# Optimization experiments

Measured on AMD Instinct MI355X. Metric: run time of the kernel, lower is better.

## Reference

```python
import jax, jax.numpy as jnp
import numpy as np

NEG_SLOPE = 0.01  # F.leaky_relu / nn.LeakyReLU default

def _leaky(x):
    return jnp.where(x >= 0, x, NEG_SLOPE * x)

def _cgconv(x, src, dst, edge_attr, Wf, bf, Ws, bs):
    # PyG CGConv: z = [x_i, x_j, e]; msg = sigmoid(lin_f(z)) * softplus(lin_s(z)); out = x + scatter_add(msg, i)
    z = jnp.concatenate([x[dst], x[src], edge_attr], axis=-1)  # [E, 2C+D]
    m = jax.nn.sigmoid(z @ Wf + bf) * jax.nn.softplus(z @ Ws + bs)  # [E, C]
    agg = jax.ops.segment_sum(m, dst, num_segments=x.shape[0])
    return x + agg

def setup_inputs() -> dict:
    key = jax.random.key(0)
    ks = jax.random.split(key, 16)
    N, E, C, D, NC, G = 50000, 800000, 128, 32, 10, 64
    inp = {}
    inp['x'] = jax.random.normal(ks[0], (N, C), dtype=jnp.float32)
    inp['y'] = jax.random.randint(ks[1], (G,), 0, NC)
    inp['edge_index'] = jax.random.randint(ks[2], (2, E), 0, N)
    inp['edge_attr'] = jax.random.normal(ks[3], (E, D), dtype=jnp.float32)
    inp['batch'] = jnp.sort(jax.random.randint(ks[4], (N,), 0, G))
    s = 0.05
    inp['lin_W'] = jax.random.normal(ks[5], (C + NC, C), dtype=jnp.float32) * s
    inp['lin_b'] = jnp.zeros((C,), dtype=jnp.float32)
    inp['c1_Wf'] = jax.random.normal(ks[6], (2 * C + D, C), dtype=jnp.float32) * s
    inp['c1_bf'] = jnp.zeros((C,), dtype=jnp.float32)
    inp['c1_Ws'] = jax.random.normal(ks[7], (2 * C + D, C), dtype=jnp.float32) * s
    inp['c1_bs'] = jnp.zeros((C,), dtype=jnp.float32)
    inp['c2_Wf'] = jax.random.normal(ks[8], (2 * C + D, C), dtype=jnp.float32) * s
    inp['c2_bf'] = jnp.zeros((C,), dtype=jnp.float32)
    inp['c2_Ws'] = jax.random.normal(ks[9], (2 * C + D, C), dtype=jnp.float32) * s
    inp['c2_bs'] = jnp.zeros((C,), dtype=jnp.float32)
    inp['fc1_W'] = jax.random.normal(ks[10], (C + NC, 32), dtype=jnp.float32) * s
    inp['fc1_b'] = jnp.zeros((32,), dtype=jnp.float32)
    inp['fc2_W'] = jax.random.normal(ks[11], (32, 1), dtype=jnp.float32) * s
    inp['fc2_b'] = jnp.zeros((1,), dtype=jnp.float32)
    return inp

def reference(x, y, edge_index, edge_attr, batch, lin_W, lin_b, c1_Wf, c1_bf, c1_Ws, c1_bs, c2_Wf, c2_bf, c2_Ws, c2_bs, fc1_W, fc1_b, fc2_W, fc2_b):
    NC = fc1_W.shape[0] - c1_Wf.shape[1]  # n_classes = 10
    G = y.shape[0]
    src, dst = edge_index[0], edge_index[1]
    one_hot = jax.nn.one_hot(y[batch], NC, dtype=x.dtype)  # [N, NC]
    h = _leaky(jnp.concatenate([x, one_hot], axis=1) @ lin_W + lin_b)
    h = _leaky(_cgconv(h, src, dst, edge_attr, c1_Wf, c1_bf, c1_Ws, c1_bs))
    h = _cgconv(h, src, dst, edge_attr, c2_Wf, c2_bf, c2_Ws, c2_bs)
    h = jnp.concatenate([h, one_hot], axis=1)  # [N, C+NC]
    sums = jax.ops.segment_sum(h, batch, num_segments=G)
    cnts = jax.ops.segment_sum(jnp.ones((h.shape[0],), h.dtype), batch, num_segments=G)
    pooled = sums / jnp.maximum(cnts, 1.0)[:, None]  # global_mean_pool
    out = _leaky(pooled @ fc1_W + fc1_b) @ fc2_W + fc2_b
    return jax.nn.sigmoid(out)
```

## Files before the change

### kernel.cpp

```cpp
#include <hip/hip_runtime.h>
#include <hip/hip_bf16.h>
#include <math.h>

#define CCH 128
#define DK  32
#define NCLS 10

typedef __attribute__((ext_vector_type(2))) float f32x2;

__device__ __forceinline__ float leaky_f(float v) { return v >= 0.f ? v : 0.01f * v; }

__global__ void k_hist(const int* __restrict__ dst, int* __restrict__ cnt, int E) {
  int e = blockIdx.x * 256 + threadIdx.x;
  if (e < E) atomicAdd(&cnt[dst[e]], 1);
}

__global__ void k_scan(const int* __restrict__ cnt, int* __restrict__ off,
                       int* __restrict__ cur, int N) {
  __shared__ int wsum[16];
  __shared__ int carry_s;
  int t = threadIdx.x;
  int lane = t & 63, w = t >> 6;
  if (t == 0) carry_s = 0;
  __syncthreads();
  for (int base = 0; base < N; base += 1024) {
    int i = base + t;
    int carry = carry_s;
    int v = (i < N) ? cnt[i] : 0;
    int s = v;
    #pragma unroll
    for (int d = 1; d < 64; d <<= 1) {
      int tmp = __shfl_up(s, d);
      if (lane >= d) s += tmp;
    }
    if (lane == 63) wsum[w] = s;
    __syncthreads();
    if (t < 16) {
      int u = wsum[t];
      #pragma unroll
      for (int d = 1; d < 16; d <<= 1) {
        int tmp = __shfl_up(u, d);
        if (t >= d) u += tmp;
      }
      wsum[t] = u;
      if (t == 15) carry_s = carry + u;
    }
    __syncthreads();
    int wbase = carry + (w > 0 ? wsum[w - 1] : 0);
    int excl = wbase + s - v;
    if (i < N) { off[i] = excl; cur[i] = excl; }
    __syncthreads();
  }
  if (t == 0) off[N] = carry_s;
}

__global__ void k_fill(const int* __restrict__ dst, const int* __restrict__ srcArr,
                       int* __restrict__ cur, int* __restrict__ eid,
                       int* __restrict__ esrc, int E) {
  int e = blockIdx.x * 256 + threadIdx.x;
  if (e < E) {
    int p = atomicAdd(&cur[dst[e]], 1);
    eid[p] = e;
    esrc[p] = srcArr[e];
  }
}

__global__ void k_gea(const int* __restrict__ eid, const float* __restrict__ ea,
                      float* __restrict__ ea_csr, int E) {
  int t = blockIdx.x * 256 + threadIdx.x;
  if (t >= E * 8) return;
  int i = t >> 3, q = t & 7;
  int e = eid[i];
  *(float4*)&ea_csr[(size_t)i * DK + q * 4] =
      *(const float4*)&ea[(size_t)e * DK + q * 4];
}

__global__ __launch_bounds__(256) void k_embed(
    const float* __restrict__ x, const float* __restrict__ lin_W,
    const float* __restrict__ lin_b, const int* __restrict__ batch,
    const int* __restrict__ y, float* __restrict__ h, int M) {
  __shared__ float Al[32 * 128];
  __shared__ float Wl[32 * 128];
  int t = threadIdx.x;
  int row0 = blockIdx.x * 32;
  for (int i = t * 4; i < 32 * 128; i += 1024) {
    int r = i >> 7, k = i & 127;
    int gr = row0 + r;
    float4 v = {0.f, 0.f, 0.f, 0.f};
    if (gr < M) v = *(const float4*)&x[(size_t)gr * 128 + k];
    *(float4*)&Al[i] = v;
  }
  int c4 = (t & 31) * 4;
  int rb = (t >> 5) * 4;
  float acc[4][4] = {};
  for (int ks = 0; ks < 128; ks += 32) {
    __syncthreads();
    for (int i = t * 4; i < 32 * 128; i += 1024)
      *(float4*)&Wl[i] = *(const float4*)&lin_W[(size_t)ks * 128 + i];
    __syncthreads();
    for (int k = 0; k < 32; k += 4) {
      float4 a[4];
      #pragma unroll
      for (int r = 0; r < 4; ++r) a[r] = *(float4*)&Al[(rb + r) * 128 + ks + k];
      #pragma unroll
      for (int kk = 0; kk < 4; ++kk) {
        float4 w = *(float4*)&Wl[(k + kk) * 128 + c4];
        #pragma unroll
        for (int r = 0; r < 4; ++r) {
          float av = kk == 0 ? a[r].x : kk == 1 ? a[r].y : kk == 2 ? a[r].z : a[r].w;
          acc[r][0] = fmaf(av, w.x, acc[r][0]);
          acc[r][1] = fmaf(av, w.y, acc[r][1]);
          acc[r][2] = fmaf(av, w.z, acc[r][2]);
          acc[r][3] = fmaf(av, w.w, acc[r][3]);
        }
      }
    }
  }
  #pragma unroll
  for (int r = 0; r < 4; ++r) {
    int gr = row0 + rb + r;
    if (gr < M) {
      int cls = y[batch[gr]];
      const float* wrow = &lin_W[(size_t)(128 + cls) * 128];
      float4 o;
      o.x = leaky_f(acc[r][0] + lin_b[c4 + 0] + wrow[c4 + 0]);
      o.y = leaky_f(acc[r][1] + lin_b[c4 + 1] + wrow[c4 + 1]);
      o.z = leaky_f(acc[r][2] + lin_b[c4 + 2] + wrow[c4 + 2]);
      o.w = leaky_f(acc[r][3] + lin_b[c4 + 3] + wrow[c4 + 3]);
      *(float4*)&h[(size_t)gr * 128 + c4] = o;
    }
  }
}

__global__ __launch_bounds__(256) void k_proj(
    const float* __restrict__ h, const float* __restrict__ Wf,
    const float* __restrict__ Ws, float* __restrict__ P, int M) {
  __shared__ float Al[32 * 128];
  __shared__ float Wl[32 * 128];
  int t = threadIdx.x;
  int part = blockIdx.y;
  const float* Wsrc = (part < 2 ? Wf : Ws) + (size_t)(part & 1) * (128 * 128);
  int row0 = blockIdx.x * 32;
  for (int i = t * 4; i < 32 * 128; i += 1024) {
    int r = i >> 7, k = i & 127;
    int gr = row0 + r;
    float4 v = {0.f, 0.f, 0.f, 0.f};
    if (gr < M) v = *(const float4*)&h[(size_t)gr * 128 + k];
    *(float4*)&Al[i] = v;
  }
  int c4 = (t & 31) * 4;
  int rb = (t >> 5) * 4;
  float acc[4][4] = {};
  for (int ks = 0; ks < 128; ks += 32) {
    __syncthreads();
    for (int i = t * 4; i < 32 * 128; i += 1024)
      *(float4*)&Wl[i] = *(const float4*)&Wsrc[(size_t)ks * 128 + i];
    __syncthreads();
    for (int k = 0; k < 32; k += 4) {
      float4 a[4];
      #pragma unroll
      for (int r = 0; r < 4; ++r) a[r] = *(float4*)&Al[(rb + r) * 128 + ks + k];
      #pragma unroll
      for (int kk = 0; kk < 4; ++kk) {
        float4 w = *(float4*)&Wl[(k + kk) * 128 + c4];
        #pragma unroll
        for (int r = 0; r < 4; ++r) {
          float av = kk == 0 ? a[r].x : kk == 1 ? a[r].y : kk == 2 ? a[r].z : a[r].w;
          acc[r][0] = fmaf(av, w.x, acc[r][0]);
          acc[r][1] = fmaf(av, w.y, acc[r][1]);
          acc[r][2] = fmaf(av, w.z, acc[r][2]);
          acc[r][3] = fmaf(av, w.w, acc[r][3]);
        }
      }
    }
  }
  #pragma unroll
  for (int r = 0; r < 4; ++r) {
    int gr = row0 + rb + r;
    if (gr < M) {
      float4 o = {acc[r][0], acc[r][1], acc[r][2], acc[r][3]};
      *(float4*)&P[(size_t)gr * 512 + part * 128 + c4] = o;
    }
  }
}

__global__ __launch_bounds__(256) __attribute__((amdgpu_waves_per_eu(3, 3)))
void k_agg(
    const float* __restrict__ hin, const float* __restrict__ P,
    const int* __restrict__ off,
    const int* __restrict__ esrcArr, const float* __restrict__ ea_csr,
    const float* __restrict__ Wf, const float* __restrict__ Ws,
    const float* __restrict__ bfv, const float* __restrict__ bsv,
    float* __restrict__ hout, int N, int do_leaky) {
  int lane = threadIdx.x & 63;
  int wave = __builtin_amdgcn_readfirstlane(threadIdx.x >> 6);
  int gw = blockIdx.x * 4 + wave;
  int c2 = lane * 2;
  f32x2 wf[DK], ws[DK];
  #pragma unroll
  for (int k = 0; k < DK; ++k) {
    wf[k] = *(const f32x2*)&Wf[(size_t)(256 + k) * 128 + c2];
    ws[k] = *(const f32x2*)&Ws[(size_t)(256 + k) * 128 + c2];
  }
  f32x2 bf2 = *(const f32x2*)&bfv[c2];
  f32x2 bs2 = *(const f32x2*)&bsv[c2];
  int nstreams = gridDim.x * 4;
  for (int n = gw; n < N; n += nstreams) {
    int i0 = __builtin_amdgcn_readfirstlane(off[n]);
    int i1 = __builtin_amdgcn_readfirstlane(off[n + 1]);
    f32x2 acc = *(const f32x2*)&hin[(size_t)n * 128 + c2];
    f32x2 gf0 = *(const f32x2*)&P[(size_t)n * 512 + c2] + bf2;
    f32x2 gs0 = *(const f32x2*)&P[(size_t)n * 512 + 256 + c2] + bs2;
    #pragma unroll 1
    for (int i = i0; i < i1; ++i) {
      int s = __builtin_amdgcn_readfirstlane(esrcArr[i]);
      f32x2 gf = gf0 + *(const f32x2*)&P[(size_t)s * 512 + 128 + c2];
      f32x2 gs = gs0 + *(const f32x2*)&P[(size_t)s * 512 + 384 + c2];
      const float4* ep4 = (const float4*)(ea_csr + (size_t)i * DK);
      #pragma unroll
      for (int q = 0; q < 4; ++q) {
        float4 a = ep4[2 * q];
        float4 b = ep4[2 * q + 1];
        float ekk[8] = {a.x, a.y, a.z, a.w, b.x, b.y, b.z, b.w};
        #pragma unroll
        for (int j = 0; j < 8; ++j) {
          int k = q * 8 + j;
          f32x2 e2 = {ekk[j], ekk[j]};
          gf += e2 * wf[k];
          gs += e2 * ws[k];
        }
      }
      float sgx = 1.f / (1.f + __expf(-gf.x));
      float sgy = 1.f / (1.f + __expf(-gf.y));
      float spx = fmaxf(gs.x, 0.f) + __logf(1.f + __expf(-fabsf(gs.x)));
      float spy = fmaxf(gs.y, 0.f) + __logf(1.f + __expf(-fabsf(gs.y)));
      acc.x = fmaf(sgx, spx, acc.x);
      acc.y = fmaf(sgy, spy, acc.y);
    }
    if (do_leaky) { acc.x = leaky_f(acc.x); acc.y = leaky_f(acc.y); }
    *(f32x2*)&hout[(size_t)n * 128 + c2] = acc;
  }
}

__device__ __forceinline__ int lbound(const int* a, int n, int key) {
  int lo = 0, hi = n;
  while (lo < hi) { int m = (lo + hi) >> 1; if (a[m] < key) lo = m + 1; else hi = m; }
  return lo;
}

__global__ void k_pool(const float* __restrict__ h, const int* __restrict__ batch,
                       float* __restrict__ pooled, int* __restrict__ gcnt, int N) {
  int g = blockIdx.x;
  int sidx = blockIdx.y, sgrid = gridDim.y;
  int t = threadIdx.x;
  int lo = lbound(batch, N, g);
  int hi = lbound(batch, N, g + 1);
  int len = hi - lo;
  if (sidx == 0 && t == 0) gcnt[g] = len;
  int per = (len + sgrid - 1) / sgrid;
  int a = lo + sidx * per;
  int b = min(hi, a + per);
  if (a >= b) return;
  float s = 0.f;
  for (int n = a; n < b; ++n) s += h[(size_t)n * 128 + t];
  atomicAdd(&pooled[g * 128 + t], s);
}

__global__ void k_fc(const float* __restrict__ pooled, const int* __restrict__ gcnt,
                     const int* __restrict__ y,
                     const float* __restrict__ W1, const float* __restrict__ b1,
                     const float* __restrict__ W2, const float* __restrict__ b2,
                     float* __restrict__ out) {
  int g = blockIdx.x;
  int j = threadIdx.x;
  float v = 0.f;
  if (j < 32) {
    int cnt = gcnt[g];
    float dot = 0.f;
    for (int k = 0; k < 128; ++k) dot = fmaf(pooled[g * 128 + k], W1[k * 32 + j], dot);
    float a = b1[j] + (cnt > 0 ? dot / (float)cnt + W1[(128 + y[g]) * 32 + j] : 0.f);
    a = leaky_f(a);
    v = a * W2[j];
  }
  #pragma unroll
  for (int o = 32; o > 0; o >>= 1) v += __shfl_down(v, o);
  if (j == 0) out[g] = 1.f / (1.f + __expf(-(v + b2[0])));
}

extern "C" void kernel_launch(void* const* d_in, const int* in_sizes, int n_in,
                              void* d_out, int out_size, void* d_ws, size_t ws_size,
                              hipStream_t stream) {
  const float* x        = (const float*)d_in[0];
  const int*   y        = (const int*)d_in[1];
  const int*   eidx     = (const int*)d_in[2];
  const float* ea       = (const float*)d_in[3];
  const int*   batch    = (const int*)d_in[4];
  const float* lin_W    = (const float*)d_in[5];
  const float* lin_b    = (const float*)d_in[6];
  const float* c1_Wf    = (const float*)d_in[7];
  const float* c1_bf    = (const float*)d_in[8];
  const float* c1_Ws    = (const float*)d_in[9];
  const float* c1_bs    = (const float*)d_in[10];
  const float* c2_Wf    = (const float*)d_in[11];
  const float* c2_bf    = (const float*)d_in[12];
  const float* c2_Ws    = (const float*)d_in[13];
  const float* c2_bs    = (const float*)d_in[14];
  const float* fc1_W    = (const float*)d_in[15];
  const float* fc1_b    = (const float*)d_in[16];
  const float* fc2_W    = (const float*)d_in[17];
  const float* fc2_b    = (const float*)d_in[18];
  float* out = (float*)d_out;

  const int N = in_sizes[0] / 128;
  const int G = in_sizes[1];
  const int E = in_sizes[2] / 2;
  const int* src = eidx;
  const int* dst = eidx + E;

  char* w = (char*)d_ws;
  float* P  = (float*)w;  w += (size_t)N * 512 * 4;
  float* hA = (float*)w;  w += (size_t)N * 128 * 4;
  float* hB = (float*)w;  w += (size_t)N * 128 * 4;
  float* pooled = (float*)w; w += (size_t)G * 128 * 4;
  int* gcnt = (int*)w; w += ((size_t)G * 4 + 15) & ~(size_t)15;
  int* cnt = (int*)w; w += (size_t)N * 4;
  int* off = (int*)w; w += ((size_t)(N + 1) * 4 + 15) & ~(size_t)15;
  int* eid = (int*)w; w += (size_t)E * 4;
  int* esrc = (int*)w; w += (size_t)E * 4;
  float* ea_csr = (float*)w; w += (size_t)E * DK * 4;

  hipMemsetAsync(cnt, 0, (size_t)N * 4, stream);
  hipMemsetAsync(pooled, 0, (size_t)G * 128 * 4, stream);
  k_hist<<<(E + 255) / 256, 256, 0, stream>>>(dst, cnt, E);
  k_scan<<<1, 1024, 0, stream>>>(cnt, off, cnt , N);
  k_fill<<<(E + 255) / 256, 256, 0, stream>>>(dst, src, cnt, eid, esrc, E);
  k_gea<<<(E * 8 + 255) / 256, 256, 0, stream>>>(eid, ea, ea_csr, E);

  k_embed<<<(N + 31) / 32, 256, 0, stream>>>(x, lin_W, lin_b, batch, y, hA, N);

  k_proj<<<dim3((N + 31) / 32, 4), 256, 0, stream>>>(hA, c1_Wf, c1_Ws, P, N);
  k_agg<<<2048, 256, 0, stream>>>(hA, P, off, esrc, ea_csr, c1_Wf, c1_Ws, c1_bf, c1_bs, hB, N, 1);

  k_proj<<<dim3((N + 31) / 32, 4), 256, 0, stream>>>(hB, c2_Wf, c2_Ws, P, N);
  k_agg<<<2048, 256, 0, stream>>>(hB, P, off, esrc, ea_csr, c2_Wf, c2_Ws, c2_bf, c2_bs, hA, N, 0);

  k_pool<<<dim3(G, 8), 128, 0, stream>>>(hA, batch, pooled, gcnt, N);
  k_fc<<<G, 64, 0, stream>>>(pooled, gcnt, y, fc1_W, fc1_b, fc2_W, fc2_b, out);
}
```

Baseline: 1.241 ms.

## Unroll edge loop by four and stream edge-weight rows from cache instead of registers

The per-node edge loop in the aggregation kernel now handles four edges at once, so each loaded edge-weight row is reused across four edges and four gathers of source rows are in flight together. The 64 edge-weight registers per lane are removed; the weights are reloaded from global memory (likely cached) on each use, and the fixed waves-per-EU attribute is dropped. This aims to raise memory-level parallelism and occupancy, at the cost of extra load traffic for the weights and a scalar tail loop for leftover edges.

Result: slower. 1.704 ms (+37.3%).

```diff
diff --git a/kernel.cpp b/kernel.cpp
--- a/kernel.cpp
+++ b/kernel.cpp
@@ -9,6 +9,15 @@
 typedef __attribute__((ext_vector_type(2))) float f32x2;
 
 __device__ __forceinline__ float leaky_f(float v) { return v >= 0.f ? v : 0.01f * v; }
+
+__device__ __forceinline__ f32x2 gate2(f32x2 gf, f32x2 gs) {
+  float sgx = 1.f / (1.f + __expf(-gf.x));
+  float sgy = 1.f / (1.f + __expf(-gf.y));
+  float spx = fmaxf(gs.x, 0.f) + __logf(1.f + __expf(-fabsf(gs.x)));
+  float spy = fmaxf(gs.y, 0.f) + __logf(1.f + __expf(-fabsf(gs.y)));
+  f32x2 r = {sgx * spx, sgy * spy};
+  return r;
+}
 
 __global__ void k_hist(const int* __restrict__ dst, int* __restrict__ cnt, int E) {
   int e = blockIdx.x * 256 + threadIdx.x;
@@ -184,7 +193,7 @@
   }
 }
 
-__global__ __launch_bounds__(256) __attribute__((amdgpu_waves_per_eu(3, 3)))
+__global__ __launch_bounds__(256)
 void k_agg(
     const float* __restrict__ hin, const float* __restrict__ P,
     const int* __restrict__ off,
@@ -196,12 +205,8 @@
   int wave = __builtin_amdgcn_readfirstlane(threadIdx.x >> 6);
   int gw = blockIdx.x * 4 + wave;
   int c2 = lane * 2;
-  f32x2 wf[DK], ws[DK];
-  #pragma unroll
-  for (int k = 0; k < DK; ++k) {
-    wf[k] = *(const f32x2*)&Wf[(size_t)(256 + k) * 128 + c2];
-    ws[k] = *(const f32x2*)&Ws[(size_t)(256 + k) * 128 + c2];
-  }
+  const float* wfp = Wf + (size_t)256 * 128 + c2;
+  const float* wsp = Ws + (size_t)256 * 128 + c2;
   f32x2 bf2 = *(const f32x2*)&bfv[c2];
   f32x2 bs2 = *(const f32x2*)&bsv[c2];
   int nstreams = gridDim.x * 4;
@@ -211,31 +216,68 @@
     f32x2 acc = *(const f32x2*)&hin[(size_t)n * 128 + c2];
     f32x2 gf0 = *(const f32x2*)&P[(size_t)n * 512 + c2] + bf2;
     f32x2 gs0 = *(const f32x2*)&P[(size_t)n * 512 + 256 + c2] + bs2;
-    #pragma unroll 1
-    for (int i = i0; i < i1; ++i) {
+    int i = i0;
+    for (; i + 4 <= i1; i += 4) {
+      int s0 = __builtin_amdgcn_readfirstlane(esrcArr[i + 0]);
+      int s1 = __builtin_amdgcn_readfirstlane(esrcArr[i + 1]);
+      int s2 = __builtin_amdgcn_readfirstlane(esrcArr[i + 2]);
+      int s3 = __builtin_amdgcn_readfirstlane(esrcArr[i + 3]);
+      f32x2 gfa = gf0 + *(const f32x2*)&P[(size_t)s0 * 512 + 128 + c2];
+      f32x2 gfb = gf0 + *(const f32x2*)&P[(size_t)s1 * 512 + 128 + c2];
+      f32x2 gfc = gf0 + *(const f32x2*)&P[(size_t)s2 * 512 + 128 + c2];
+      f32x2 gfd = gf0 + *(const f32x2*)&P[(size_t)s3 * 512 + 128 + c2];
+      f32x2 gsa = gs0 + *(const f32x2*)&P[(size_t)s0 * 512 + 384 + c2];
+      f32x2 gsb = gs0 + *(const f32x2*)&P[(size_t)s1 * 512 + 384 + c2];
+      f32x2 gsc = gs0 + *(const f32x2*)&P[(size_t)s2 * 512 + 384 + c2];
+      f32x2 gsd = gs0 + *(const f32x2*)&P[(size_t)s3 * 512 + 384 + c2];
+      const float* e0 = ea_csr + (size_t)i * DK;
+      #pragma unroll
+      for (int q = 0; q < 8; ++q) {
+        float4 ev0 = *(const float4*)&e0[q * 4];
+        float4 ev1 = *(const float4*)&e0[DK + q * 4];
+        float4 ev2 = *(const float4*)&e0[2 * DK + q * 4];
+        float4 ev3 = *(const float4*)&e0[3 * DK + q * 4];
+        #pragma unroll
+        for (int j = 0; j < 4; ++j) {
+          int k = q * 4 + j;
+          f32x2 wfk = *(const f32x2*)&wfp[(size_t)k * 128];
+          f32x2 wsk = *(const f32x2*)&wsp[(size_t)k * 128];
+          float a = j == 0 ? ev0.x : j == 1 ? ev0.y : j == 2 ? ev0.z : ev0.w;
+          float b = j == 0 ? ev1.x : j == 1 ? ev1.y : j == 2 ? ev1.z : ev1.w;
+          float c = j == 0 ? ev2.x : j == 1 ? ev2.y : j == 2 ? ev2.z : ev2.w;
+          float d = j == 0 ? ev3.x : j == 1 ? ev3.y : j == 2 ? ev3.z : ev3.w;
+          f32x2 a2 = {a, a}, b2 = {b, b}, c2v = {c, c}, d2 = {d, d};
+          gfa += a2 * wfk; gsa += a2 * wsk;
+          gfb += b2 * wfk; gsb += b2 * wsk;
+          gfc += c2v * wfk; gsc += c2v * wsk;
+          gfd += d2 * wfk; gsd += d2 * wsk;
+        }
+      }
+      acc += gate2(gfa, gsa);
+      acc += gate2(gfb, gsb);
+      acc += gate2(gfc, gsc);
+      acc += gate2(gfd, gsd);
+    }
+    for (; i < i1; ++i) {
       int s = __builtin_amdgcn_readfirstlane(esrcArr[i]);
       f32x2 gf = gf0 + *(const f32x2*)&P[(size_t)s * 512 + 128 + c2];
       f32x2 gs = gs0 + *(const f32x2*)&P[(size_t)s * 512 + 384 + c2];
-      const float4* ep4 = (const float4*)(ea_csr + (size_t)i * DK);
-      #pragma unroll
-      for (int q = 0; q < 4; ++q) {
-        float4 a = ep4[2 * q];
-        float4 b = ep4[2 * q + 1];
-        float ekk[8] = {a.x, a.y, a.z, a.w, b.x, b.y, b.z, b.w};
+      const float* e0 = ea_csr + (size_t)i * DK;
+      #pragma unroll
+      for (int q = 0; q < 8; ++q) {
+        float4 ev = *(const float4*)&e0[q * 4];
         #pragma unroll
-        for (int j = 0; j < 8; ++j) {
-          int k = q * 8 + j;
-          f32x2 e2 = {ekk[j], ekk[j]};
-          gf += e2 * wf[k];
-          gs += e2 * ws[k];
+        for (int j = 0; j < 4; ++j) {
+          int k = q * 4 + j;
+          f32x2 wfk = *(const f32x2*)&wfp[(size_t)k * 128];
+          f32x2 wsk = *(const f32x2*)&wsp[(size_t)k * 128];
+          float e = j == 0 ? ev.x : j == 1 ? ev.y : j == 2 ? ev.z : ev.w;
+          f32x2 e2 = {e, e};
+          gf += e2 * wfk;
+          gs += e2 * wsk;
         }
       }
-      float sgx = 1.f / (1.f + __expf(-gf.x));
-      float sgy = 1.f / (1.f + __expf(-gf.y));
-      float spx = fmaxf(gs.x, 0.f) + __logf(1.f + __expf(-fabsf(gs.x)));
-      float spy = fmaxf(gs.y, 0.f) + __logf(1.f + __expf(-fabsf(gs.y)));
-      acc.x = fmaf(sgx, spx, acc.x);
-      acc.y = fmaf(sgy, spy, acc.y);
+      acc += gate2(gf, gs);
     }
     if (do_leaky) { acc.x = leaky_f(acc.x); acc.y = leaky_f(acc.y); }
     *(f32x2*)&hout[(size_t)n * 128 + c2] = acc;
```

## Move edge-attr weight slices from registers to LDS to raise occupancy

Applied to the files above, without the earlier changes.

The per-lane edge-attribute weight columns (Wf/Ws rows 256..287), previously held in 128 VGPRs, are now staged once per block into 32 KB of shared memory and read from LDS inside the edge loop. Launch bounds change from a fixed 3 waves/EU to a request for higher occupancy, so more waves can hide the latency of gathering P rows. The trade is extra LDS reads per edge (64 per lane per edge) and an LDS footprint that may itself cap resident blocks. The gate math is moved into a helper with unchanged semantics apart from a separate multiply and add instead of fmaf.

Result: no change. 1.240 ms (-0.2%).

```diff
diff --git a/kernel.cpp b/kernel.cpp
--- a/kernel.cpp
+++ b/kernel.cpp
@@ -9,6 +9,15 @@
 typedef __attribute__((ext_vector_type(2))) float f32x2;
 
 __device__ __forceinline__ float leaky_f(float v) { return v >= 0.f ? v : 0.01f * v; }
+
+__device__ __forceinline__ f32x2 gate2(f32x2 gf, f32x2 gs) {
+  float sgx = 1.f / (1.f + __expf(-gf.x));
+  float sgy = 1.f / (1.f + __expf(-gf.y));
+  float spx = fmaxf(gs.x, 0.f) + __logf(1.f + __expf(-fabsf(gs.x)));
+  float spy = fmaxf(gs.y, 0.f) + __logf(1.f + __expf(-fabsf(gs.y)));
+  f32x2 r = {sgx * spx, sgy * spy};
+  return r;
+}
 
 __global__ void k_hist(const int* __restrict__ dst, int* __restrict__ cnt, int E) {
   int e = blockIdx.x * 256 + threadIdx.x;
@@ -184,7 +193,7 @@
   }
 }
 
-__global__ __launch_bounds__(256) __attribute__((amdgpu_waves_per_eu(3, 3)))
+__global__ __launch_bounds__(256, 8)
 void k_agg(
     const float* __restrict__ hin, const float* __restrict__ P,
     const int* __restrict__ off,
@@ -192,16 +201,18 @@
     const float* __restrict__ Wf, const float* __restrict__ Ws,
     const float* __restrict__ bfv, const float* __restrict__ bsv,
     float* __restrict__ hout, int N, int do_leaky) {
-  int lane = threadIdx.x & 63;
-  int wave = __builtin_amdgcn_readfirstlane(threadIdx.x >> 6);
+  __shared__ float WlF[32 * 128];
+  __shared__ float WlS[32 * 128];
+  int t = threadIdx.x;
+  for (int i = t * 4; i < 32 * 128; i += 1024) {
+    *(float4*)&WlF[i] = *(const float4*)&Wf[(size_t)256 * 128 + i];
+    *(float4*)&WlS[i] = *(const float4*)&Ws[(size_t)256 * 128 + i];
+  }
+  __syncthreads();
+  int lane = t & 63;
+  int wave = __builtin_amdgcn_readfirstlane(t >> 6);
   int gw = blockIdx.x * 4 + wave;
   int c2 = lane * 2;
-  f32x2 wf[DK], ws[DK];
-  #pragma unroll
-  for (int k = 0; k < DK; ++k) {
-    wf[k] = *(const f32x2*)&Wf[(size_t)(256 + k) * 128 + c2];
-    ws[k] = *(const f32x2*)&Ws[(size_t)(256 + k) * 128 + c2];
-  }
   f32x2 bf2 = *(const f32x2*)&bfv[c2];
   f32x2 bs2 = *(const f32x2*)&bsv[c2];
   int nstreams = gridDim.x * 4;
@@ -216,26 +227,23 @@
       int s = __builtin_amdgcn_readfirstlane(esrcArr[i]);
       f32x2 gf = gf0 + *(const f32x2*)&P[(size_t)s * 512 + 128 + c2];
       f32x2 gs = gs0 + *(const f32x2*)&P[(size_t)s * 512 + 384 + c2];
-      const float4* ep4 = (const float4*)(ea_csr + (size_t)i * DK);
+      const float* e0 = ea_csr + (size_t)i * DK;
       #pragma unroll
       for (int q = 0; q < 4; ++q) {
-        float4 a = ep4[2 * q];
-        float4 b = ep4[2 * q + 1];
+        float4 a = *(const float4*)&e0[q * 8];
+        float4 b = *(const float4*)&e0[q * 8 + 4];
         float ekk[8] = {a.x, a.y, a.z, a.w, b.x, b.y, b.z, b.w};
         #pragma unroll
         for (int j = 0; j < 8; ++j) {
           int k = q * 8 + j;
+          f32x2 wfk = *(const f32x2*)&WlF[k * 128 + c2];
+          f32x2 wsk = *(const f32x2*)&WlS[k * 128 + c2];
           f32x2 e2 = {ekk[j], ekk[j]};
-          gf += e2 * wf[k];
-          gs += e2 * ws[k];
+          gf += e2 * wfk;
+          gs += e2 * wsk;
         }
       }
-      float sgx = 1.f / (1.f + __expf(-gf.x));
-      float sgy = 1.f / (1.f + __expf(-gf.y));
-      float spx = fmaxf(gs.x, 0.f) + __logf(1.f + __expf(-fabsf(gs.x)));
-      float spy = fmaxf(gs.y, 0.f) + __logf(1.f + __expf(-fabsf(gs.y)));
-      acc.x = fmaf(sgx, spx, acc.x);
-      acc.y = fmaf(sgy, spy, acc.y);
+      acc += gate2(gf, gs);
     }
     if (do_leaky) { acc.x = leaky_f(acc.x); acc.y = leaky_f(acc.y); }
     *(f32x2*)&hout[(size_t)n * 128 + c2] = acc;
```
